# Kernel optimization log

Measured on AMD Instinct MI355X. Metric: run time of the kernel, lower is better.

The kernel has to match this reference:

```python
import jax, jax.numpy as jnp
import numpy as np

EMBED_DIM = 1024
NUM_HEADS = 16
HEAD_DIM = EMBED_DIM // NUM_HEADS
B, S = 2, 2048


def setup_inputs() -> dict:
    key = jax.random.key(0)
    ks = jax.random.split(key, 11)
    init = 0.02
    return {
        "query": jax.random.normal(ks[0], (B, S, EMBED_DIM), jnp.float32),
        "key": jax.random.normal(ks[1], (B, S, EMBED_DIM), jnp.float32),
        "value": jax.random.normal(ks[2], (B, S, EMBED_DIM), jnp.float32),
        "Wq": jax.random.normal(ks[3], (EMBED_DIM, EMBED_DIM), jnp.float32) * init,
        "bq": jnp.zeros((EMBED_DIM,), jnp.float32),
        "Wk": jax.random.normal(ks[4], (EMBED_DIM, EMBED_DIM), jnp.float32) * init,
        "bk": jnp.zeros((EMBED_DIM,), jnp.float32),
        "Wv": jax.random.normal(ks[5], (EMBED_DIM, EMBED_DIM), jnp.float32) * init,
        "bv": jnp.zeros((EMBED_DIM,), jnp.float32),
        "Wo": jax.random.normal(ks[6], (EMBED_DIM, EMBED_DIM), jnp.float32) * init,
        "bo": jnp.zeros((EMBED_DIM,), jnp.float32),
    }


def reference(query, key, value, Wq, bq, Wk, bk, Wv, bv, Wo, bo):
    scale = jnp.sqrt(jnp.asarray(HEAD_DIM, query.dtype))
    # projections (torch Linear: x @ W.T + b)
    Q = query @ Wq.T + bq
    K = key @ Wk.T + bk
    V = value @ Wv.T + bv
    # [B, S, E] -> [B, H, S, D]
    def split_heads(x):
        return x.reshape(B, -1, NUM_HEADS, HEAD_DIM).transpose(0, 2, 1, 3)
    Qh, Kh, Vh = split_heads(Q), split_heads(K), split_heads(V)
    # scores: [B, H, S, S] -- the O(N^2) intermediate
    scores = jnp.einsum("bhqd,bhkd->bhqk", Qh, Kh) / scale
    attn_weights = jax.nn.softmax(scores, axis=-1)
    # dropout = 0.0 (eval mode)
    out = jnp.einsum("bhqk,bhkd->bhqd", attn_weights, Vh)
    out = out.transpose(0, 2, 1, 3).reshape(B, -1, EMBED_DIM)
    output = out @ Wo.T + bo
    return output, attn_weights
```

## Files before the change

### kernel.cpp

```cpp
#include <hip/hip_runtime.h>
#include <hip/hip_bf16.h>

typedef unsigned short u16;
typedef u16 u16x8 __attribute__((ext_vector_type(8)));
typedef u16 u16x4 __attribute__((ext_vector_type(4)));
typedef __bf16 bf16x8 __attribute__((ext_vector_type(8)));
typedef float f32x4 __attribute__((ext_vector_type(4)));

#define B_ 2
#define S_ 2048
#define E_ 1024
#define H_ 16
#define D_ 64
#define QSCALE 0.18033688011112042f

__device__ __forceinline__ u16 f2bf(float f) {
    return __builtin_bit_cast(u16, static_cast<__bf16>(f));
}
__device__ __forceinline__ float bf2f(unsigned u) {
    return __builtin_bit_cast(float, u << 16);
}

__device__ __forceinline__ void glds16(const u16* g, u16* l) {
    __builtin_amdgcn_global_load_lds(
        (const __attribute__((address_space(1))) unsigned int*)g,
        (__attribute__((address_space(3))) unsigned int*)l, 16, 0, 0);
}

#define VMCNT0 asm volatile("s_waitcnt vmcnt(0)" ::: "memory")
#define RAW_BAR() do { __builtin_amdgcn_s_barrier(); asm volatile("" ::: "memory"); } while (0)

__device__ __forceinline__ bf16x8 lds_read8(const u16* base, int row, int k) {
    const char* p = (const char*)base + (((row * 128) + (k * 2)) ^ ((row & 7) << 4));
    return __builtin_bit_cast(bf16x8, *(const u16x8*)p);
}

__device__ __forceinline__ f32x4 mfma16x16(bf16x8 a, bf16x8 b, f32x4 c) {
    return __builtin_amdgcn_mfma_f32_16x16x32_bf16(a, b, c, 0, 0, 0);
}

__global__ __launch_bounds__(256) void cvt_kernel(const float* __restrict__ q,
                                                  const float* __restrict__ k,
                                                  const float* __restrict__ v,
                                                  const float* __restrict__ wq,
                                                  const float* __restrict__ wk,
                                                  const float* __restrict__ wv,
                                                  const float* __restrict__ wo,
                                                  u16* __restrict__ qkv_dst,
                                                  u16* __restrict__ w_dst) {
    const int bid = blockIdx.x;
    const float* src;
    u16* dst;
    if (bid < 6144) {
        const int t = bid >> 11, lb = bid & 2047;
        src = (t == 0 ? q : t == 1 ? k : v) + (size_t)lb * 2048;
        dst = qkv_dst + (size_t)t * 4194304 + (size_t)lb * 2048;
    } else {
        const int t = (bid - 6144) >> 9, lb = (bid - 6144) & 511;
        src = (t == 0 ? wq : t == 1 ? wk : t == 2 ? wv : wo) + (size_t)lb * 2048;
        dst = w_dst + (size_t)t * 1048576 + (size_t)lb * 2048;
    }
    const int off = threadIdx.x * 8;
    f32x4 a = *(const f32x4*)(src + off);
    f32x4 b = *(const f32x4*)(src + off + 4);
    u16x8 o;
#pragma unroll
    for (int i = 0; i < 4; ++i) { o[i] = f2bf(a[i]); o[4 + i] = f2bf(b[i]); }
    *(u16x8*)(dst + off) = o;
}

__global__ __launch_bounds__(256) void gemm_qkv(const u16* __restrict__ qkv_bf,
                                                const u16* __restrict__ w_bf,
                                                const float* __restrict__ bq,
                                                const float* __restrict__ bk,
                                                const float* __restrict__ bv,
                                                u16* __restrict__ outbase) {
    const int z = blockIdx.z;
    const u16* A = qkv_bf + (size_t)z * 4194304;
    const u16* W = w_bf + (size_t)z * 1048576;
    const float* bias = (z == 0) ? bq : (z == 1) ? bk : bv;
    u16* outp = outbase + (size_t)z * 4194304;

    const int n0 = blockIdx.x * 128;
    const int m0 = blockIdx.y * 128;
    const int tid = threadIdx.x;
    const int lane = tid & 63, g = lane >> 4, c = lane & 15;
    const int w = tid >> 6, wm = w >> 1, wn = w & 1;

    __shared__ u16 lA[2][8192];
    __shared__ u16 lB[2][8192];

    auto stage = [&](int buf, int kt) {
#pragma unroll
        for (int i = 0; i < 4; ++i) {
            const int chunk = (w * 4 + i) * 64 + lane;
            const int r = chunk >> 3, sg = chunk & 7, ss = sg ^ (r & 7);
            glds16(A + (size_t)(m0 + r) * 1024 + kt * 64 + ss * 8, &lA[buf][(w * 4 + i) * 512]);
            glds16(W + (size_t)(n0 + r) * 1024 + kt * 64 + ss * 8, &lB[buf][(w * 4 + i) * 512]);
        }
    };

    f32x4 acc[4][4] = {};
    stage(0, 0);
    VMCNT0;
    __syncthreads();

    for (int kt = 0; kt < 16; ++kt) {
        const int buf = kt & 1;
        if (kt < 15) stage(buf ^ 1, kt + 1);
#pragma unroll
        for (int ks = 0; ks < 2; ++ks) {
            bf16x8 af[4], bfr[4];
#pragma unroll
            for (int fm = 0; fm < 4; ++fm) af[fm] = lds_read8(lA[buf], wm * 64 + fm * 16 + c, g * 8 + ks * 32);
#pragma unroll
            for (int fn = 0; fn < 4; ++fn) bfr[fn] = lds_read8(lB[buf], wn * 64 + fn * 16 + c, g * 8 + ks * 32);
#pragma unroll
            for (int fm = 0; fm < 4; ++fm)
#pragma unroll
                for (int fn = 0; fn < 4; ++fn)
                    acc[fm][fn] = mfma16x16(af[fm], bfr[fn], acc[fm][fn]);
        }
        VMCNT0;
        RAW_BAR();
    }

    float bv_[4];
#pragma unroll
    for (int fn = 0; fn < 4; ++fn) bv_[fn] = bias[n0 + wn * 64 + fn * 16 + c];

#pragma unroll
    for (int fm = 0; fm < 4; ++fm) {
#pragma unroll
        for (int fn = 0; fn < 4; ++fn) {
            const int mbase = m0 + wm * 64 + fm * 16 + g * 4;
            const int n = n0 + wn * 64 + fn * 16 + c;
            if (z == 2) {
                u16x4 vv;
#pragma unroll
                for (int r = 0; r < 4; ++r) vv[r] = f2bf(acc[fm][fn][r] + bv_[fn]);
                const int b = mbase >> 11, s = mbase & 2047, h = n >> 6, d = n & 63;
                u16* dst = outp + ((size_t)((b * 16 + h) * 64 + d)) * 2048 + s;
                *(u16x4*)dst = vv;
            } else {
                const float sc = (z == 0) ? QSCALE : 1.0f;
#pragma unroll
                for (int r = 0; r < 4; ++r) {
                    const float val = (acc[fm][fn][r] + bv_[fn]) * sc;
                    const int m = mbase + r;
                    const int b = m >> 11, s = m & 2047, h = n >> 6, d = n & 63;
                    outp[((size_t)((b * 16 + h) * 2048 + s)) * 64 + d] = f2bf(val);
                }
            }
        }
    }
}

__global__ __launch_bounds__(256) void gemm_out(const u16* __restrict__ A,
                                                const u16* __restrict__ W,
                                                const float* __restrict__ bias,
                                                float* __restrict__ outp) {
    const int n0 = blockIdx.x * 128;
    const int m0 = blockIdx.y * 128;
    const int tid = threadIdx.x;
    const int lane = tid & 63, g = lane >> 4, c = lane & 15;
    const int w = tid >> 6, wm = w >> 1, wn = w & 1;

    __shared__ u16 lA[2][8192];
    __shared__ u16 lB[2][8192];

    auto stage = [&](int buf, int kt) {
#pragma unroll
        for (int i = 0; i < 4; ++i) {
            const int chunk = (w * 4 + i) * 64 + lane;
            const int r = chunk >> 3, sg = chunk & 7, ss = sg ^ (r & 7);
            glds16(A + (size_t)(m0 + r) * 1024 + kt * 64 + ss * 8, &lA[buf][(w * 4 + i) * 512]);
            glds16(W + (size_t)(n0 + r) * 1024 + kt * 64 + ss * 8, &lB[buf][(w * 4 + i) * 512]);
        }
    };

    f32x4 acc[4][4] = {};
    stage(0, 0);
    VMCNT0;
    __syncthreads();

    for (int kt = 0; kt < 16; ++kt) {
        const int buf = kt & 1;
        if (kt < 15) stage(buf ^ 1, kt + 1);
#pragma unroll
        for (int ks = 0; ks < 2; ++ks) {
            bf16x8 af[4], bfr[4];
#pragma unroll
            for (int fm = 0; fm < 4; ++fm) af[fm] = lds_read8(lA[buf], wm * 64 + fm * 16 + c, g * 8 + ks * 32);
#pragma unroll
            for (int fn = 0; fn < 4; ++fn) bfr[fn] = lds_read8(lB[buf], wn * 64 + fn * 16 + c, g * 8 + ks * 32);
#pragma unroll
            for (int fm = 0; fm < 4; ++fm)
#pragma unroll
                for (int fn = 0; fn < 4; ++fn)
                    acc[fm][fn] = mfma16x16(af[fm], bfr[fn], acc[fm][fn]);
        }
        VMCNT0;
        RAW_BAR();
    }

    float bv_[4];
#pragma unroll
    for (int fn = 0; fn < 4; ++fn) bv_[fn] = bias[n0 + wn * 64 + fn * 16 + c];

#pragma unroll
    for (int fm = 0; fm < 4; ++fm)
#pragma unroll
        for (int fn = 0; fn < 4; ++fn) {
            const int mbase = m0 + wm * 64 + fm * 16 + g * 4;
            const int n = n0 + wn * 64 + fn * 16 + c;
#pragma unroll
            for (int r = 0; r < 4; ++r)
                outp[(size_t)(mbase + r) * 1024 + n] = acc[fm][fn][r] + bv_[fn];
        }
}

__global__ __launch_bounds__(256) void attn_kernel(const u16* __restrict__ Qh,
                                                   const u16* __restrict__ Kh,
                                                   const u16* __restrict__ Vt,
                                                   float* __restrict__ attnW,
                                                   u16* __restrict__ Obf) {
    const int bid = blockIdx.x;
    const int sw = ((bid & 7) << 6) + (bid >> 3);
    const int bh = sw >> 4, qt = sw & 15;
    const int tid = threadIdx.x;
    const int lane = tid & 63, g = lane >> 4, c = lane & 15;
    const int w = tid >> 6;

    __shared__ u16 lQ[8192];
    __shared__ u16 lKV[2][8192];
    __shared__ u16 lP[4][2048];

    const u16* Qbase = Qh + ((size_t)bh * S_ + qt * 128) * D_;
    const u16* Kbase = Kh + (size_t)bh * S_ * D_;
    const u16* Vbase = Vt + (size_t)bh * D_ * S_;

#pragma unroll
    for (int i = 0; i < 4; ++i) {
        const int chunk = (w * 4 + i) * 64 + lane;
        const int r = chunk >> 3, sg = chunk & 7, ss = sg ^ (r & 7);
        glds16(Qbase + r * 64 + ss * 8, &lQ[(w * 4 + i) * 512]);
    }
    auto stageK128 = [&](int buf, int kt2) {
#pragma unroll
        for (int i = 0; i < 4; ++i) {
            const int chunk = (w * 4 + i) * 64 + lane;
            const int r = chunk >> 3, sg = chunk & 7, ss = sg ^ (r & 7);
            glds16(Kbase + (size_t)(kt2 * 128 + r) * 64 + ss * 8, &lKV[buf][(w * 4 + i) * 512]);
        }
    };
    auto stageKV64 = [&](int buf, int kt) {
#pragma unroll
        for (int i = 0; i < 2; ++i) {
            const int chunk = (w * 2 + i) * 64 + lane;
            const int r = chunk >> 3, sg = chunk & 7, ss = sg ^ (r & 7);
            glds16(Kbase + (size_t)(kt * 64 + r) * 64 + ss * 8, &lKV[buf][(w * 2 + i) * 512]);
            glds16(Vbase + (size_t)r * S_ + kt * 64 + ss * 8, &lKV[buf][4096 + (w * 2 + i) * 512]);
        }
    };

    stageK128(0, 0);
    VMCNT0;
    __syncthreads();

    float l_run[2] = {0.f, 0.f};

    for (int kt2 = 0; kt2 < 16; ++kt2) {
        const int buf = kt2 & 1;
        if (kt2 < 15) stageK128(buf ^ 1, kt2 + 1);

#pragma unroll
        for (int sub = 0; sub < 2; ++sub) {
            f32x4 s[4][2] = {};
            __builtin_amdgcn_s_setprio(1);
#pragma unroll
            for (int ks = 0; ks < 2; ++ks) {
                bf16x8 a[4], b[2];
#pragma unroll
                for (int kf = 0; kf < 4; ++kf) a[kf] = lds_read8(lKV[buf], sub * 64 + kf * 16 + c, g * 8 + ks * 32);
#pragma unroll
                for (int qf = 0; qf < 2; ++qf) b[qf] = lds_read8(lQ, w * 32 + qf * 16 + c, g * 8 + ks * 32);
#pragma unroll
                for (int kf = 0; kf < 4; ++kf)
#pragma unroll
                    for (int qf = 0; qf < 2; ++qf)
                        s[kf][qf] = mfma16x16(a[kf], b[qf], s[kf][qf]);
            }
            __builtin_amdgcn_s_setprio(0);
#pragma unroll
            for (int qf = 0; qf < 2; ++qf) {
                float ts = 0.f;
#pragma unroll
                for (int kf = 0; kf < 4; ++kf)
#pragma unroll
                    for (int r = 0; r < 4; ++r) ts += exp2f(s[kf][qf][r]);
                ts += __shfl_xor(ts, 16);
                ts += __shfl_xor(ts, 32);
                l_run[qf] += ts;
            }
        }
        VMCNT0;
        RAW_BAR();
    }
    const float linv[2] = {1.f / l_run[0], 1.f / l_run[1]};

    f32x4 o[2][4] = {};
    stageKV64(0, 0);
    VMCNT0;
    RAW_BAR();

    for (int kt = 0; kt < 32; ++kt) {
        const int buf = kt & 1;
        if (kt < 31) stageKV64(buf ^ 1, kt + 1);

        f32x4 s[4][2] = {};
        __builtin_amdgcn_s_setprio(1);
#pragma unroll
        for (int ks = 0; ks < 2; ++ks) {
            bf16x8 a[4], b[2];
#pragma unroll
            for (int kf = 0; kf < 4; ++kf) a[kf] = lds_read8(lKV[buf], kf * 16 + c, g * 8 + ks * 32);
#pragma unroll
            for (int qf = 0; qf < 2; ++qf) b[qf] = lds_read8(lQ, w * 32 + qf * 16 + c, g * 8 + ks * 32);
#pragma unroll
            for (int kf = 0; kf < 4; ++kf)
#pragma unroll
                for (int qf = 0; qf < 2; ++qf)
                    s[kf][qf] = mfma16x16(a[kf], b[qf], s[kf][qf]);
        }
        __builtin_amdgcn_s_setprio(0);

        u16* myP = lP[w];
#pragma unroll
        for (int qf = 0; qf < 2; ++qf) {
#pragma unroll
            for (int kf = 0; kf < 4; ++kf) {
                f32x4 p4;
#pragma unroll
                for (int r = 0; r < 4; ++r) p4[r] = exp2f(s[kf][qf][r]) * linv[qf];
#pragma unroll
                for (int rp = 0; rp < 2; ++rp) {
                    const unsigned pk = (unsigned)f2bf(p4[2 * rp]) |
                                        ((unsigned)f2bf(p4[2 * rp + 1]) << 16);
                    const int row = qf * 16 + c;
                    const int col = kf * 16 + g * 4 + 2 * rp;
                    *(unsigned*)((char*)myP + (((row * 128) + (col * 2)) ^ ((row & 7) << 4))) = pk;
                }
            }
        }

        __builtin_amdgcn_s_setprio(1);
#pragma unroll
        for (int ks = 0; ks < 2; ++ks) {
            bf16x8 pa[2], vb[4];
#pragma unroll
            for (int fm = 0; fm < 2; ++fm) pa[fm] = lds_read8(myP, fm * 16 + c, g * 8 + ks * 32);
#pragma unroll
            for (int fn = 0; fn < 4; ++fn) vb[fn] = lds_read8(lKV[buf] + 4096, fn * 16 + c, g * 8 + ks * 32);
#pragma unroll
            for (int fm = 0; fm < 2; ++fm)
#pragma unroll
                for (int fn = 0; fn < 4; ++fn)
                    o[fm][fn] = mfma16x16(pa[fm], vb[fn], o[fm][fn]);
        }
        __builtin_amdgcn_s_setprio(0);

        {
            const size_t qbase = (size_t)bh * S_ + (size_t)(qt * 128 + w * 32);
#pragma unroll
            for (int j = 0; j < 8; ++j) {
                const int row = j * 4 + g;
                const unsigned long long pv8 = *(const unsigned long long*)(
                    (const char*)myP + (((row * 128) + c * 8) ^ ((row & 7) << 4)));
                f32x4 o4;
                o4[0] = bf2f((unsigned)(pv8 & 0xffffu));
                o4[1] = bf2f((unsigned)((pv8 >> 16) & 0xffffu));
                o4[2] = bf2f((unsigned)((pv8 >> 32) & 0xffffu));
                o4[3] = bf2f((unsigned)((pv8 >> 48) & 0xffffu));
                __builtin_nontemporal_store(
                    o4, (f32x4*)(attnW + (qbase + row) * S_ + kt * 64 + c * 4));
            }
        }

        asm volatile("s_waitcnt vmcnt(8)" ::: "memory");
        RAW_BAR();
    }

    const int b2 = bh >> 4, h = bh & 15;
#pragma unroll
    for (int fm = 0; fm < 2; ++fm)
#pragma unroll
        for (int fn = 0; fn < 4; ++fn)
#pragma unroll
            for (int r = 0; r < 4; ++r) {
                const int q = qt * 128 + w * 32 + fm * 16 + g * 4 + r;
                const int d = fn * 16 + c;
                __builtin_nontemporal_store(
                    f2bf(o[fm][fn][r]),
                    &Obf[((size_t)(b2 * S_ + q)) * E_ + h * 64 + d]);
            }
}

extern "C" void kernel_launch(void* const* d_in, const int* in_sizes, int n_in,
                              void* d_out, int out_size, void* d_ws, size_t ws_size,
                              hipStream_t stream) {
    const float* query = (const float*)d_in[0];
    const float* key_ = (const float*)d_in[1];
    const float* value = (const float*)d_in[2];
    const float* Wq = (const float*)d_in[3];
    const float* bq = (const float*)d_in[4];
    const float* Wk = (const float*)d_in[5];
    const float* bk = (const float*)d_in[6];
    const float* Wv = (const float*)d_in[7];
    const float* bv = (const float*)d_in[8];
    const float* Wo = (const float*)d_in[9];
    const float* bo = (const float*)d_in[10];

    u16* qkv_bf = (u16*)d_ws;
    u16* w_bf = qkv_bf + (size_t)12 * 1024 * 1024;
    u16* Qh = qkv_bf + (size_t)16 * 1024 * 1024;
    u16* Obf = qkv_bf;

    float* out0 = (float*)d_out;
    float* attnW = out0 + (size_t)B_ * S_ * E_;

    cvt_kernel<<<8192, 256, 0, stream>>>(query, key_, value, Wq, Wk, Wv, Wo, qkv_bf, w_bf);

    gemm_qkv<<<dim3(8, 32, 3), 256, 0, stream>>>(qkv_bf, w_bf, bq, bk, bv, Qh);

    attn_kernel<<<512, 256, 0, stream>>>(Qh, Qh + (size_t)4 * 1024 * 1024,
                                         Qh + (size_t)8 * 1024 * 1024, attnW, Obf);

    gemm_out<<<dim3(8, 32), 256, 0, stream>>>(Obf, w_bf + (size_t)3 * 1024 * 1024, bo, (float*)d_out);
}
```

Baseline: 234.0 us.

## Halve attention query tile to 64 rows and hold Q fragments in registers

```diff
diff --git a/kernel.cpp b/kernel.cpp
--- a/kernel.cpp
+++ b/kernel.cpp
@@ -226,26 +226,25 @@
                                                    float* __restrict__ attnW,
                                                    u16* __restrict__ Obf) {
     const int bid = blockIdx.x;
-    const int sw = ((bid & 7) << 6) + (bid >> 3);
-    const int bh = sw >> 4, qt = sw & 15;
+    const int sw = ((bid & 7) << 7) + (bid >> 3);
+    const int bh = sw >> 5, qt = sw & 31;
     const int tid = threadIdx.x;
     const int lane = tid & 63, g = lane >> 4, c = lane & 15;
     const int w = tid >> 6;
 
-    __shared__ u16 lQ[8192];
     __shared__ u16 lKV[2][8192];
-    __shared__ u16 lP[4][2048];
-
-    const u16* Qbase = Qh + ((size_t)bh * S_ + qt * 128) * D_;
+    __shared__ u16 lP[4][1024];
+
+    const u16* Qbase = Qh + ((size_t)bh * S_ + qt * 64) * D_;
     const u16* Kbase = Kh + (size_t)bh * S_ * D_;
     const u16* Vbase = Vt + (size_t)bh * D_ * S_;
 
-#pragma unroll
-    for (int i = 0; i < 4; ++i) {
-        const int chunk = (w * 4 + i) * 64 + lane;
-        const int r = chunk >> 3, sg = chunk & 7, ss = sg ^ (r & 7);
-        glds16(Qbase + r * 64 + ss * 8, &lQ[(w * 4 + i) * 512]);
-    }
+    bf16x8 qreg[2];
+#pragma unroll
+    for (int ks = 0; ks < 2; ++ks)
+        qreg[ks] = __builtin_bit_cast(bf16x8,
+            *(const u16x8*)(Qbase + (size_t)(w * 16 + c) * 64 + ks * 32 + g * 8));
+
     auto stageK128 = [&](int buf, int kt2) {
 #pragma unroll
         for (int i = 0; i < 4; ++i) {
@@ -268,7 +267,7 @@
     VMCNT0;
     __syncthreads();
 
-    float l_run[2] = {0.f, 0.f};
+    float l_run = 0.f;
 
     for (int kt2 = 0; kt2 < 16; ++kt2) {
         const int buf = kt2 & 1;
@@ -276,40 +275,34 @@
 
 #pragma unroll
         for (int sub = 0; sub < 2; ++sub) {
-            f32x4 s[4][2] = {};
+            f32x4 s[4] = {};
             __builtin_amdgcn_s_setprio(1);
 #pragma unroll
             for (int ks = 0; ks < 2; ++ks) {
-                bf16x8 a[4], b[2];
-#pragma unroll
-                for (int kf = 0; kf < 4; ++kf) a[kf] = lds_read8(lKV[buf], sub * 64 + kf * 16 + c, g * 8 + ks * 32);
-#pragma unroll
-                for (int qf = 0; qf < 2; ++qf) b[qf] = lds_read8(lQ, w * 32 + qf * 16 + c, g * 8 + ks * 32);
+                bf16x8 a[4];
 #pragma unroll
                 for (int kf = 0; kf < 4; ++kf)
-#pragma unroll
-                    for (int qf = 0; qf < 2; ++qf)
-                        s[kf][qf] = mfma16x16(a[kf], b[qf], s[kf][qf]);
+                    a[kf] = lds_read8(lKV[buf], sub * 64 + kf * 16 + c, g * 8 + ks * 32);
+#pragma unroll
+                for (int kf = 0; kf < 4; ++kf)
+                    s[kf] = mfma16x16(a[kf], qreg[ks], s[kf]);
             }
             __builtin_amdgcn_s_setprio(0);
-#pragma unroll
-            for (int qf = 0; qf < 2; ++qf) {
-                float ts = 0.f;
-#pragma unroll
-                for (int kf = 0; kf < 4; ++kf)
-#pragma unroll
-                    for (int r = 0; r < 4; ++r) ts += exp2f(s[kf][qf][r]);
-                ts += __shfl_xor(ts, 16);
-                ts += __shfl_xor(ts, 32);
-                l_run[qf] += ts;
-            }
+            float ts = 0.f;
+#pragma unroll
+            for (int kf = 0; kf < 4; ++kf)
+#pragma unroll
+                for (int r = 0; r < 4; ++r) ts += exp2f(s[kf][r]);
+            ts += __shfl_xor(ts, 16);
+            ts += __shfl_xor(ts, 32);
+            l_run += ts;
         }
         VMCNT0;
         RAW_BAR();
     }
-    const float linv[2] = {1.f / l_run[0], 1.f / l_run[1]};
-
-    f32x4 o[2][4] = {};
+    const float linv = 1.f / l_run;
+
+    f32x4 o[4] = {};
     stageKV64(0, 0);
     VMCNT0;
     RAW_BAR();
@@ -318,62 +311,54 @@
         const int buf = kt & 1;
         if (kt < 31) stageKV64(buf ^ 1, kt + 1);
 
-        f32x4 s[4][2] = {};
+        f32x4 s[4] = {};
         __builtin_amdgcn_s_setprio(1);
 #pragma unroll
         for (int ks = 0; ks < 2; ++ks) {
-            bf16x8 a[4], b[2];
-#pragma unroll
-            for (int kf = 0; kf < 4; ++kf) a[kf] = lds_read8(lKV[buf], kf * 16 + c, g * 8 + ks * 32);
-#pragma unroll
-            for (int qf = 0; qf < 2; ++qf) b[qf] = lds_read8(lQ, w * 32 + qf * 16 + c, g * 8 + ks * 32);
+            bf16x8 a[4];
 #pragma unroll
             for (int kf = 0; kf < 4; ++kf)
-#pragma unroll
-                for (int qf = 0; qf < 2; ++qf)
-                    s[kf][qf] = mfma16x16(a[kf], b[qf], s[kf][qf]);
+                a[kf] = lds_read8(lKV[buf], kf * 16 + c, g * 8 + ks * 32);
+#pragma unroll
+            for (int kf = 0; kf < 4; ++kf)
+                s[kf] = mfma16x16(a[kf], qreg[ks], s[kf]);
         }
         __builtin_amdgcn_s_setprio(0);
 
         u16* myP = lP[w];
 #pragma unroll
-        for (int qf = 0; qf < 2; ++qf) {
-#pragma unroll
-            for (int kf = 0; kf < 4; ++kf) {
-                f32x4 p4;
-#pragma unroll
-                for (int r = 0; r < 4; ++r) p4[r] = exp2f(s[kf][qf][r]) * linv[qf];
-#pragma unroll
-                for (int rp = 0; rp < 2; ++rp) {
-                    const unsigned pk = (unsigned)f2bf(p4[2 * rp]) |
-                                        ((unsigned)f2bf(p4[2 * rp + 1]) << 16);
-                    const int row = qf * 16 + c;
-                    const int col = kf * 16 + g * 4 + 2 * rp;
-                    *(unsigned*)((char*)myP + (((row * 128) + (col * 2)) ^ ((row & 7) << 4))) = pk;
-                }
+        for (int kf = 0; kf < 4; ++kf) {
+            f32x4 p4;
+#pragma unroll
+            for (int r = 0; r < 4; ++r) p4[r] = exp2f(s[kf][r]) * linv;
+#pragma unroll
+            for (int rp = 0; rp < 2; ++rp) {
+                const unsigned pk = (unsigned)f2bf(p4[2 * rp]) |
+                                    ((unsigned)f2bf(p4[2 * rp + 1]) << 16);
+                const int row = c;
+                const int col = kf * 16 + g * 4 + 2 * rp;
+                *(unsigned*)((char*)myP + (((row * 128) + (col * 2)) ^ ((row & 7) << 4))) = pk;
             }
         }
 
         __builtin_amdgcn_s_setprio(1);
 #pragma unroll
         for (int ks = 0; ks < 2; ++ks) {
-            bf16x8 pa[2], vb[4];
-#pragma unroll
-            for (int fm = 0; fm < 2; ++fm) pa[fm] = lds_read8(myP, fm * 16 + c, g * 8 + ks * 32);
-#pragma unroll
-            for (int fn = 0; fn < 4; ++fn) vb[fn] = lds_read8(lKV[buf] + 4096, fn * 16 + c, g * 8 + ks * 32);
-#pragma unroll
-            for (int fm = 0; fm < 2; ++fm)
-#pragma unroll
-                for (int fn = 0; fn < 4; ++fn)
-                    o[fm][fn] = mfma16x16(pa[fm], vb[fn], o[fm][fn]);
+            bf16x8 pa = lds_read8(myP, c, g * 8 + ks * 32);
+            bf16x8 vb[4];
+#pragma unroll
+            for (int fn = 0; fn < 4; ++fn)
+                vb[fn] = lds_read8(lKV[buf] + 4096, fn * 16 + c, g * 8 + ks * 32);
+#pragma unroll
+            for (int fn = 0; fn < 4; ++fn)
+                o[fn] = mfma16x16(pa, vb[fn], o[fn]);
         }
         __builtin_amdgcn_s_setprio(0);
 
         {
-            const size_t qbase = (size_t)bh * S_ + (size_t)(qt * 128 + w * 32);
-#pragma unroll
-            for (int j = 0; j < 8; ++j) {
+            const size_t qbase = (size_t)bh * S_ + (size_t)(qt * 64 + w * 16);
+#pragma unroll
+            for (int j = 0; j < 4; ++j) {
                 const int row = j * 4 + g;
                 const unsigned long long pv8 = *(const unsigned long long*)(
                     (const char*)myP + (((row * 128) + c * 8) ^ ((row & 7) << 4)));
@@ -387,23 +372,21 @@
             }
         }
 
-        asm volatile("s_waitcnt vmcnt(8)" ::: "memory");
+        asm volatile("s_waitcnt vmcnt(4)" ::: "memory");
         RAW_BAR();
     }
 
     const int b2 = bh >> 4, h = bh & 15;
 #pragma unroll
-    for (int fm = 0; fm < 2; ++fm)
-#pragma unroll
-        for (int fn = 0; fn < 4; ++fn)
-#pragma unroll
-            for (int r = 0; r < 4; ++r) {
-                const int q = qt * 128 + w * 32 + fm * 16 + g * 4 + r;
-                const int d = fn * 16 + c;
-                __builtin_nontemporal_store(
-                    f2bf(o[fm][fn][r]),
-                    &Obf[((size_t)(b2 * S_ + q)) * E_ + h * 64 + d]);
-            }
+    for (int fn = 0; fn < 4; ++fn)
+#pragma unroll
+        for (int r = 0; r < 4; ++r) {
+            const int q = qt * 64 + w * 16 + g * 4 + r;
+            const int d = fn * 16 + c;
+            __builtin_nontemporal_store(
+                f2bf(o[fn][r]),
+                &Obf[((size_t)(b2 * S_ + q)) * E_ + h * 64 + d]);
+        }
 }
 
 extern "C" void kernel_launch(void* const* d_in, const int* in_sizes, int n_in,
@@ -433,8 +416,8 @@
 
     gemm_qkv<<<dim3(8, 32, 3), 256, 0, stream>>>(qkv_bf, w_bf, bq, bk, bv, Qh);
 
-    attn_kernel<<<512, 256, 0, stream>>>(Qh, Qh + (size_t)4 * 1024 * 1024,
-                                         Qh + (size_t)8 * 1024 * 1024, attnW, Obf);
+    attn_kernel<<<1024, 256, 0, stream>>>(Qh, Qh + (size_t)4 * 1024 * 1024,
+                                          Qh + (size_t)8 * 1024 * 1024, attnW, Obf);
 
     gemm_out<<<dim3(8, 32), 256, 0, stream>>>(Obf, w_bf + (size_t)3 * 1024 * 1024, bo, (float*)d_out);
 }
```

After: 244.1 us. +4.3%, slower.

## Keep Q fragments in registers, drop Q LDS tile, reorder PV after stores

Applied to the files above, without the earlier changes.

```diff
diff --git a/kernel.cpp b/kernel.cpp
--- a/kernel.cpp
+++ b/kernel.cpp
@@ -220,11 +220,11 @@
         }
 }
 
-__global__ __launch_bounds__(256) void attn_kernel(const u16* __restrict__ Qh,
-                                                   const u16* __restrict__ Kh,
-                                                   const u16* __restrict__ Vt,
-                                                   float* __restrict__ attnW,
-                                                   u16* __restrict__ Obf) {
+__global__ __launch_bounds__(256, 3) void attn_kernel(const u16* __restrict__ Qh,
+                                                      const u16* __restrict__ Kh,
+                                                      const u16* __restrict__ Vt,
+                                                      float* __restrict__ attnW,
+                                                      u16* __restrict__ Obf) {
     const int bid = blockIdx.x;
     const int sw = ((bid & 7) << 6) + (bid >> 3);
     const int bh = sw >> 4, qt = sw & 15;
@@ -232,7 +232,6 @@
     const int lane = tid & 63, g = lane >> 4, c = lane & 15;
     const int w = tid >> 6;
 
-    __shared__ u16 lQ[8192];
     __shared__ u16 lKV[2][8192];
     __shared__ u16 lP[4][2048];
 
@@ -240,12 +239,14 @@
     const u16* Kbase = Kh + (size_t)bh * S_ * D_;
     const u16* Vbase = Vt + (size_t)bh * D_ * S_;
 
-#pragma unroll
-    for (int i = 0; i < 4; ++i) {
-        const int chunk = (w * 4 + i) * 64 + lane;
-        const int r = chunk >> 3, sg = chunk & 7, ss = sg ^ (r & 7);
-        glds16(Qbase + r * 64 + ss * 8, &lQ[(w * 4 + i) * 512]);
-    }
+    bf16x8 qreg[2][2];
+#pragma unroll
+    for (int qf = 0; qf < 2; ++qf)
+#pragma unroll
+        for (int ks = 0; ks < 2; ++ks)
+            qreg[qf][ks] = __builtin_bit_cast(bf16x8,
+                *(const u16x8*)(Qbase + (size_t)(w * 32 + qf * 16 + c) * 64 + ks * 32 + g * 8));
+
     auto stageK128 = [&](int buf, int kt2) {
 #pragma unroll
         for (int i = 0; i < 4; ++i) {
@@ -280,16 +281,15 @@
             __builtin_amdgcn_s_setprio(1);
 #pragma unroll
             for (int ks = 0; ks < 2; ++ks) {
-                bf16x8 a[4], b[2];
-#pragma unroll
-                for (int kf = 0; kf < 4; ++kf) a[kf] = lds_read8(lKV[buf], sub * 64 + kf * 16 + c, g * 8 + ks * 32);
-#pragma unroll
-                for (int qf = 0; qf < 2; ++qf) b[qf] = lds_read8(lQ, w * 32 + qf * 16 + c, g * 8 + ks * 32);
+                bf16x8 a[4];
 #pragma unroll
                 for (int kf = 0; kf < 4; ++kf)
+                    a[kf] = lds_read8(lKV[buf], sub * 64 + kf * 16 + c, g * 8 + ks * 32);
+#pragma unroll
+                for (int kf = 0; kf < 4; ++kf)
 #pragma unroll
                     for (int qf = 0; qf < 2; ++qf)
-                        s[kf][qf] = mfma16x16(a[kf], b[qf], s[kf][qf]);
+                        s[kf][qf] = mfma16x16(a[kf], qreg[qf][ks], s[kf][qf]);
             }
             __builtin_amdgcn_s_setprio(0);
 #pragma unroll
@@ -322,16 +322,15 @@
         __builtin_amdgcn_s_setprio(1);
 #pragma unroll
         for (int ks = 0; ks < 2; ++ks) {
-            bf16x8 a[4], b[2];
-#pragma unroll
-            for (int kf = 0; kf < 4; ++kf) a[kf] = lds_read8(lKV[buf], kf * 16 + c, g * 8 + ks * 32);
-#pragma unroll
-            for (int qf = 0; qf < 2; ++qf) b[qf] = lds_read8(lQ, w * 32 + qf * 16 + c, g * 8 + ks * 32);
+            bf16x8 a[4];
 #pragma unroll
             for (int kf = 0; kf < 4; ++kf)
+                a[kf] = lds_read8(lKV[buf], kf * 16 + c, g * 8 + ks * 32);
+#pragma unroll
+            for (int kf = 0; kf < 4; ++kf)
 #pragma unroll
                 for (int qf = 0; qf < 2; ++qf)
-                    s[kf][qf] = mfma16x16(a[kf], b[qf], s[kf][qf]);
+                    s[kf][qf] = mfma16x16(a[kf], qreg[qf][ks], s[kf][qf]);
         }
         __builtin_amdgcn_s_setprio(0);
 
@@ -353,22 +352,6 @@
                 }
             }
         }
-
-        __builtin_amdgcn_s_setprio(1);
-#pragma unroll
-        for (int ks = 0; ks < 2; ++ks) {
-            bf16x8 pa[2], vb[4];
-#pragma unroll
-            for (int fm = 0; fm < 2; ++fm) pa[fm] = lds_read8(myP, fm * 16 + c, g * 8 + ks * 32);
-#pragma unroll
-            for (int fn = 0; fn < 4; ++fn) vb[fn] = lds_read8(lKV[buf] + 4096, fn * 16 + c, g * 8 + ks * 32);
-#pragma unroll
-            for (int fm = 0; fm < 2; ++fm)
-#pragma unroll
-                for (int fn = 0; fn < 4; ++fn)
-                    o[fm][fn] = mfma16x16(pa[fm], vb[fn], o[fm][fn]);
-        }
-        __builtin_amdgcn_s_setprio(0);
 
         {
             const size_t qbase = (size_t)bh * S_ + (size_t)(qt * 128 + w * 32);
@@ -382,10 +365,25 @@
                 o4[1] = bf2f((unsigned)((pv8 >> 16) & 0xffffu));
                 o4[2] = bf2f((unsigned)((pv8 >> 32) & 0xffffu));
                 o4[3] = bf2f((unsigned)((pv8 >> 48) & 0xffffu));
-                __builtin_nontemporal_store(
-                    o4, (f32x4*)(attnW + (qbase + row) * S_ + kt * 64 + c * 4));
-            }
-        }
+                *(f32x4*)(attnW + (qbase + row) * S_ + kt * 64 + c * 4) = o4;
+            }
+        }
+
+        __builtin_amdgcn_s_setprio(1);
+#pragma unroll
+        for (int ks = 0; ks < 2; ++ks) {
+            bf16x8 pa[2], vb[4];
+#pragma unroll
+            for (int fm = 0; fm < 2; ++fm) pa[fm] = lds_read8(myP, fm * 16 + c, g * 8 + ks * 32);
+#pragma unroll
+            for (int fn = 0; fn < 4; ++fn) vb[fn] = lds_read8(lKV[buf] + 4096, fn * 16 + c, g * 8 + ks * 32);
+#pragma unroll
+            for (int fm = 0; fm < 2; ++fm)
+#pragma unroll
+                for (int fn = 0; fn < 4; ++fn)
+                    o[fm][fn] = mfma16x16(pa[fm], vb[fn], o[fm][fn]);
+        }
+        __builtin_amdgcn_s_setprio(0);
 
         asm volatile("s_waitcnt vmcnt(8)" ::: "memory");
         RAW_BAR();
@@ -400,9 +398,7 @@
             for (int r = 0; r < 4; ++r) {
                 const int q = qt * 128 + w * 32 + fm * 16 + g * 4 + r;
                 const int d = fn * 16 + c;
-                __builtin_nontemporal_store(
-                    f2bf(o[fm][fn][r]),
-                    &Obf[((size_t)(b2 * S_ + q)) * E_ + h * 64 + d]);
+                Obf[((size_t)(b2 * S_ + q)) * E_ + h * 64 + d] = f2bf(o[fm][fn][r]);
             }
 }
 
```

Measured after the change: 288.8 us. 23.4% more time.
